# Kernel optimization log

Hardware: AMD Instinct MI355X
Metric: run time of the kernel (lower is better)

Reference implementation:

```python
import jax, jax.numpy as jnp
import numpy as np

N, X_DIM, Y_DIM, HID = 8192, 512, 2048 // 4, 2048
Y_DIM = 512

def setup_inputs() -> dict:
    key = jax.random.key(0)
    ks = jax.random.split(key, 10)
    def lin(k, fan_in, fan_out):
        lim = 1.0 / np.sqrt(fan_in)
        kw, kb = jax.random.split(k)
        W = jax.random.uniform(kw, (fan_in, fan_out), jnp.float32, -lim, lim)
        b = jax.random.uniform(kb, (fan_out,), jnp.float32, -lim, lim)
        return W, b
    mu_W1, mu_b1 = lin(ks[0], X_DIM, HID)
    mu_W2, mu_b2 = lin(ks[1], HID, Y_DIM)
    lv_W1, lv_b1 = lin(ks[2], X_DIM, HID)
    lv_W2, lv_b2 = lin(ks[3], HID, Y_DIM)
    return {
        "x_samples": jax.random.normal(ks[4], (N, X_DIM), jnp.float32),
        "y_samples": jax.random.normal(ks[5], (N, Y_DIM), jnp.float32),
        "mu_W1": mu_W1, "mu_b1": mu_b1, "mu_W2": mu_W2, "mu_b2": mu_b2,
        "lv_W1": lv_W1, "lv_b1": lv_b1, "lv_W2": lv_W2, "lv_b2": lv_b2,
    }

def reference(x_samples, y_samples, mu_W1, mu_b1, mu_W2, mu_b2, lv_W1, lv_b1, lv_W2, lv_b2):
    # MLP heads (GEMMs)
    mu = jax.nn.relu(x_samples @ mu_W1 + mu_b1) @ mu_W2 + mu_b2          # [N, D]
    logvar = jnp.tanh(jax.nn.relu(x_samples @ lv_W1 + lv_b1) @ lv_W2 + lv_b2)  # [N, D]
    w = 0.5 * jnp.exp(-logvar)                                           # 1/(2*exp(logvar))
    n = x_samples.shape[0]

    # positive: -mean_i sum_d (mu_id - y_id)^2 * w_id
    positive = -(((mu - y_samples) ** 2) * w).sum(axis=1).mean()

    # negative (exact decomposition of the [N,N,D] broadcast):
    # -(1/N^2) sum_{i,d} w_id * (N*mu_id^2 - 2*mu_id*Sy_d + Sy2_d)
    Sy = y_samples.sum(axis=0)          # [D]
    Sy2 = (y_samples ** 2).sum(axis=0)  # [D]
    negative = -(w * (n * mu ** 2 - 2.0 * mu * Sy + Sy2)).sum() / (n * n)

    return positive - negative
```

## Files before the change

### kernel.cpp

```cpp
#include <hip/hip_runtime.h>
#include <hip/hip_bf16.h>
#include <stdint.h>

#define NS   8192
#define XD   512
#define HD   2048
#define YD   512

typedef unsigned short u16;
using bf16x8 = __attribute__((ext_vector_type(8))) short;
using f32x4  = __attribute__((ext_vector_type(4))) float;

__device__ __forceinline__ float bf2f(u16 u) {
  union { uint32_t i; float f; } v; v.i = ((uint32_t)u) << 16; return v.f;
}
__device__ __forceinline__ u16 f2b(float f) {
  __hip_bfloat16 hb = __float2bfloat16(f);
  return *(const u16*)&hb;
}
__device__ __forceinline__ float ld_in(const void* p, int f32, size_t i) {
  return f32 ? ((const float*)p)[i] : bf2f(((const u16*)p)[i]);
}
#define GLDS(gp, lp) __builtin_amdgcn_global_load_lds( \
    (__attribute__((address_space(1))) void*)(gp),     \
    (__attribute__((address_space(3))) void*)(lp), 16, 0, 0)

__device__ __forceinline__ int probe_f32(const void* p, int n_u16, int* sflag) {
  if (threadIdx.x == 0) *sflag = 0;
  __syncthreads();
  const u16* q = (const u16*)p;
  int wild = 0;
  for (int i = threadIdx.x; i < n_u16; i += blockDim.x) {
    float v = bf2f(q[i]);
    if (!(fabsf(v) <= 1000.0f)) wild = 1;
  }
  if (wild) *sflag = 1;
  __syncthreads();
  int r = *sflag;
  __syncthreads();
  return r;
}

__global__ __launch_bounds__(256) void prep_all(
    const void* __restrict__ x,
    const void* w1m, const void* b1m, const void* w2m, const void* b2m,
    const void* w1l, const void* b1l, const void* w2l, const void* b2l,
    const void* __restrict__ y,
    u16* __restrict__ xb, float* __restrict__ biasv,
    u16* __restrict__ W1t, u16* __restrict__ W2tm, u16* __restrict__ W2tl,
    float* __restrict__ Sy, float* __restrict__ Sy2) {
  __shared__ u16 tile[64 * 72];
  __shared__ int sflag;
  const int b = blockIdx.x;
  const int tid = threadIdx.x;

  if (b < 2048) {
    if (!probe_f32(x, 1024, &sflag)) return;
    const size_t base = (size_t)b * 2048 + (size_t)tid * 8;
    alignas(16) u16 o[8];
    const float4* s = (const float4*)((const float*)x + base);
    float4 v0 = s[0], v1 = s[1];
    o[0]=f2b(v0.x); o[1]=f2b(v0.y); o[2]=f2b(v0.z); o[3]=f2b(v0.w);
    o[4]=f2b(v1.x); o[5]=f2b(v1.y); o[6]=f2b(v1.z); o[7]=f2b(v1.w);
    *(uint4*)(xb + base) = *(const uint4*)o;
  } else if (b == 2048) {
    const int f3 = probe_f32(b1m, 1024, &sflag);
    const int f5 = probe_f32(b2m, 512, &sflag);
    const int f7 = probe_f32(b1l, 1024, &sflag);
    const int f9 = probe_f32(b2l, 512, &sflag);
    for (int i = tid; i < 5120; i += 256) {
      float v;
      if (i < 2048)      v = ld_in(b1m, f3, i);
      else if (i < 4096) v = ld_in(b1l, f7, i - 2048);
      else if (i < 4608) v = ld_in(b2m, f5, i - 4096);
      else               v = ld_in(b2l, f9, i - 4608);
      biasv[i] = v;
    }
  } else if (b < 3073) {
    const int id = b - 2049, which = id >> 8, t = id & 255;
    const void* in; u16* out; int R, C;
    if (which == 0)      { in = w1m; out = W1t;                   R = XD; C = HD; }
    else if (which == 1) { in = w2m; out = W2tm;                  R = HD; C = YD; }
    else if (which == 2) { in = w1l; out = W1t + (size_t)HD * XD; R = XD; C = HD; }
    else                 { in = w2l; out = W2tl;                  R = HD; C = YD; }
    const int f = probe_f32(in, 1024, &sflag);
    const int nbx = C >> 6;
    const int c0 = (t % nbx) * 64, r0 = (t / nbx) * 64;
    const int r = tid >> 2, cc = (tid & 3) * 16;
    if (f) {
      const float4* s = (const float4*)((const float*)in + (size_t)(r0 + r) * C + c0 + cc);
#pragma unroll
      for (int k = 0; k < 4; ++k) {
        float4 v = s[k];
        tile[r * 72 + cc + k * 4 + 0] = f2b(v.x);
        tile[r * 72 + cc + k * 4 + 1] = f2b(v.y);
        tile[r * 72 + cc + k * 4 + 2] = f2b(v.z);
        tile[r * 72 + cc + k * 4 + 3] = f2b(v.w);
      }
    } else {
      const uint4* s = (const uint4*)((const u16*)in + (size_t)(r0 + r) * C + c0 + cc);
      *(uint4*)&tile[r * 72 + cc]     = s[0];
      *(uint4*)&tile[r * 72 + cc + 8] = s[1];
    }
    __syncthreads();
    const int i = tid >> 2, jc = (tid & 3) * 16;
    alignas(16) u16 o[16];
#pragma unroll
    for (int j = 0; j < 16; ++j) o[j] = tile[(jc + j) * 72 + i];
    uint4* dq = (uint4*)&out[(size_t)(c0 + i) * R + r0 + jc];
    dq[0] = ((const uint4*)o)[0];
    dq[1] = ((const uint4*)o)[1];
  } else {
    const int id2 = b - 3073;
    const int yf = probe_f32(y, 1024, &sflag);
    const int half = tid >> 7;
    const int c0 = (tid & 127) * 4;
    const int r0 = id2 * 128 + half * 64;
    float s0 = 0.f, s1 = 0.f, s2 = 0.f, s3 = 0.f;
    float q0 = 0.f, q1 = 0.f, q2 = 0.f, q3 = 0.f;
    for (int r = r0; r < r0 + 64; r += 4) {
#pragma unroll
      for (int rr = 0; rr < 4; ++rr) {
        float v0, v1, v2, v3;
        if (yf) {
          const float4 t4 = *(const float4*)((const float*)y + (size_t)(r + rr) * YD + c0);
          v0 = t4.x; v1 = t4.y; v2 = t4.z; v3 = t4.w;
        } else {
          const uint2 t2 = *(const uint2*)((const u16*)y + (size_t)(r + rr) * YD + c0);
          v0 = bf2f((u16)(t2.x & 0xffff)); v1 = bf2f((u16)(t2.x >> 16));
          v2 = bf2f((u16)(t2.y & 0xffff)); v3 = bf2f((u16)(t2.y >> 16));
        }
        s0 += v0; q0 += v0 * v0;  s1 += v1; q1 += v1 * v1;
        s2 += v2; q2 += v2 * v2;  s3 += v3; q3 += v3 * v3;
      }
    }
    atomicAdd(&Sy[c0],     s0);  atomicAdd(&Sy2[c0],     q0);
    atomicAdd(&Sy[c0 + 1], s1);  atomicAdd(&Sy2[c0 + 1], q1);
    atomicAdd(&Sy[c0 + 2], s2);  atomicAdd(&Sy2[c0 + 2], q2);
    atomicAdd(&Sy[c0 + 3], s3);  atomicAdd(&Sy2[c0 + 3], q3);
  }
}

#define SYNC_PRE do { \
  __builtin_amdgcn_sched_barrier(0); \
  __builtin_amdgcn_s_barrier(); \
  asm volatile("s_waitcnt lgkmcnt(0)" ::: "memory"); \
  __builtin_amdgcn_sched_barrier(0); \
  __builtin_amdgcn_s_setprio(1); } while (0)
#define SYNC_POST do { \
  __builtin_amdgcn_s_setprio(0); \
  __builtin_amdgcn_sched_barrier(0); \
  __builtin_amdgcn_s_barrier(); \
  __builtin_amdgcn_sched_barrier(0); } while (0)
#define VMCNT(N) asm volatile("s_waitcnt vmcnt(" #N ")" ::: "memory")
#define LGKM0 asm volatile("s_waitcnt lgkmcnt(0)" ::: "memory")
#define SCB __builtin_amdgcn_sched_barrier(0)

#define RD_A(MH, BUF) do { \
  const u16* ab_ = &lds[((BUF)*2 + wm) * 8192]; \
  _Pragma("unroll") for (int q_ = 0; q_ < 4; ++q_) \
    _Pragma("unroll") for (int ks_ = 0; ks_ < 2; ++ks_) \
      af[q_][ks_] = *(const bf16x8*)&ab_[((MH)*64 + q_*16 + c16)*64 + (((ks_*4+quad) ^ cswz) << 3)]; \
} while (0)

#define RD_B(NH, BUF) do { \
  const u16* bb_ = &lds[32768 + ((BUF)*2 + (wn>>1)) * 8192]; \
  _Pragma("unroll") for (int p_ = 0; p_ < 2; ++p_) \
    _Pragma("unroll") for (int ks_ = 0; ks_ < 2; ++ks_) \
      bf[(NH)*2+p_][ks_] = *(const bf16x8*)&bb_[((wn&1)*64 + ((NH)*2+p_)*16 + c16)*64 + (((ks_*4+quad) ^ cswz) << 3)]; \
} while (0)

#define MM(MH, NH) do { \
  _Pragma("unroll") for (int ks_ = 0; ks_ < 2; ++ks_) \
    _Pragma("unroll") for (int q_ = 0; q_ < 4; ++q_) \
      _Pragma("unroll") for (int p_ = 0; p_ < 2; ++p_) \
        acc[(MH)*4+q_][(NH)*2+p_] = __builtin_amdgcn_mfma_f32_16x16x32_bf16( \
            af[q_][ks_], bf[(NH)*2+p_][ks_], acc[(MH)*4+q_][(NH)*2+p_], 0, 0, 0); \
} while (0)

#define ST_A(KT, HALF) do { if ((KT) < 8) { \
  u16* lb_ = &lds[(((KT)&1)*2 + (HALF))*8192 + (wid << 9)]; \
  const u16* sp_ = Aptr + (size_t)(bm0 + (HALF)*128 + (wid<<3) + srow)*512 + ((KT)<<6) + scg; \
  GLDS(sp_, lb_); GLDS(sp_ + (size_t)64*512, lb_ + 4096); } } while (0)

#define ST_B(KT, HALF) do { if ((KT) < 8) { \
  u16* lb_ = &lds[32768 + (((KT)&1)*2 + (HALF))*8192 + (wid << 9)]; \
  const u16* sp_ = W1t + (size_t)(bn0 + (HALF)*128 + (wid<<3) + srow)*512 + ((KT)<<6) + scg; \
  GLDS(sp_, lb_); GLDS(sp_ + (size_t)64*512, lb_ + 4096); } } while (0)

__global__ __launch_bounds__(512, 2) void gemm1_kernel(
    const void* __restrict__ xraw, const u16* __restrict__ xb,
    const u16* __restrict__ W1t,
    const float* __restrict__ bias,
    u16* __restrict__ h_mu, u16* __restrict__ h_lv) {
  __shared__ alignas(16) u16 lds[65536];
  __shared__ int sflag;
  const int tid = threadIdx.x;

  const u16* Aptr = probe_f32(xraw, 1024, &sflag) ? xb : (const u16*)xraw;

  const int wid = tid >> 6, lane = tid & 63;
  const int wm = wid >> 2, wn = wid & 3;
  const int quad = lane >> 4, c16 = lane & 15, cswz = c16 & 7;
  const int srow = lane >> 3;
  const int scg  = ((lane & 7) ^ srow) << 3;

  const int id = blockIdx.x;
  const int xcd = id & 7, slot = id >> 3;
  const int bm0 = (xcd * 4 + (slot & 3)) * 256;
  const int bn0 = (slot >> 2) * 256;

  f32x4 acc[8][4] = {};
  bf16x8 af[4][2], bf[4][2];

  ST_B(0, 0); ST_B(0, 1); ST_A(0, 0); ST_A(0, 1);
  ST_B(1, 0); ST_B(1, 1);
  VMCNT(4);
  __builtin_amdgcn_s_barrier();
  __builtin_amdgcn_sched_barrier(0);

#pragma unroll
  for (int i = 0; i < 4; ++i) {
    const int ka = 2 * i, kb = ka + 1;
    const bool last = (i == 3);
    RD_A(0, 0); RD_B(0, 0); ST_A(kb, 0);
    SYNC_PRE; MM(0, 0); SYNC_POST;
    RD_B(1, 0); ST_A(kb, 1);
    SYNC_PRE; MM(0, 1); SYNC_POST;
    RD_A(1, 0); ST_B(ka + 2, 0);
    SYNC_PRE; MM(1, 0); SYNC_POST;
    ST_B(ka + 2, 1);
    SYNC_PRE; MM(1, 1);
    if (!last) { VMCNT(4); } else { VMCNT(0); }
    SYNC_POST;
    RD_A(0, 1); RD_B(0, 1); ST_A(ka + 2, 0);
    SYNC_PRE; MM(0, 0); SYNC_POST;
    RD_B(1, 1); ST_A(ka + 2, 1);
    SYNC_PRE; MM(0, 1); SYNC_POST;
    RD_A(1, 1); ST_B(kb + 2, 0);
    SYNC_PRE; MM(1, 0); SYNC_POST;
    ST_B(kb + 2, 1);
    SYNC_PRE; MM(1, 1);
    if (!last) { VMCNT(4); }
    SYNC_POST;
  }

  u16* myl = &lds[wid * 8192];
  const bool is_lv = bn0 >= HD;
  u16* dst = is_lv ? h_lv : h_mu;
  const int wncol = wn << 6;
  const int gc0 = (bn0 - (is_lv ? HD : 0)) + wncol;
  const int grow0 = bm0 + (wm << 7);
#pragma unroll
  for (int ni = 0; ni < 4; ++ni) {
    const float bv = bias[bn0 + wncol + ni * 16 + c16];
#pragma unroll
    for (int mi = 0; mi < 8; ++mi)
#pragma unroll
      for (int r = 0; r < 4; ++r) {
        const int row = mi * 16 + (quad << 2) + r;
        const int col = ni * 16 + c16;
        myl[row * 64 + ((((col >> 3) ^ (row & 7)) << 3) | (col & 7))] =
            f2b(fmaxf(acc[mi][ni][r] + bv, 0.f));
      }
  }
#pragma unroll
  for (int it = 0; it < 16; ++it) {
    const int row = (it << 3) + (lane >> 3);
    const int ch = lane & 7;
    const uint4 v = *(const uint4*)&myl[row * 64 + ((ch ^ (row & 7)) << 3)];
    *(uint4*)&dst[(size_t)(grow0 + row) * HD + gc0 + (ch << 3)] = v;
  }
}

#undef RD_A
#undef RD_B
#undef MM
#undef ST_A
#undef ST_B

#define LDA8(AF, T) do { \
  const uint64_t o_ = (uint64_t)(T) * 128u; \
  asm volatile("global_load_dwordx4 %0, %1, off"           : "=v"(AF[0][0]) : "v"(aA[0] + o_)); \
  asm volatile("global_load_dwordx4 %0, %1, off offset:64" : "=v"(AF[0][1]) : "v"(aA[0] + o_)); \
  asm volatile("global_load_dwordx4 %0, %1, off"           : "=v"(AF[1][0]) : "v"(aA[1] + o_)); \
  asm volatile("global_load_dwordx4 %0, %1, off offset:64" : "=v"(AF[1][1]) : "v"(aA[1] + o_)); \
  asm volatile("global_load_dwordx4 %0, %1, off"           : "=v"(AF[2][0]) : "v"(aA[2] + o_)); \
  asm volatile("global_load_dwordx4 %0, %1, off offset:64" : "=v"(AF[2][1]) : "v"(aA[2] + o_)); \
  asm volatile("global_load_dwordx4 %0, %1, off"           : "=v"(AF[3][0]) : "v"(aA[3] + o_)); \
  asm volatile("global_load_dwordx4 %0, %1, off offset:64" : "=v"(AF[3][1]) : "v"(aA[3] + o_)); \
} while (0)

#define RD8(BUFI) do { \
  _Pragma("unroll") for (int ni_ = 0; ni_ < 4; ++ni_) \
    _Pragma("unroll") for (int ks_ = 0; ks_ < 2; ++ks_) \
      bf[ni_][ks_] = *(const bf16x8*)&lds[(BUFI)*16384 + rbase + \
          (wn*64 + ni_*16 + c16)*64 + (((ks_*4+quad) ^ cswz) << 3)]; \
} while (0)

#define MM32(AF) do { \
  _Pragma("unroll") for (int ks_ = 0; ks_ < 2; ++ks_) \
    _Pragma("unroll") for (int mi_ = 0; mi_ < 4; ++mi_) \
      _Pragma("unroll") for (int ni_ = 0; ni_ < 4; ++ni_) \
        acc[mi_][ni_] = __builtin_amdgcn_mfma_f32_16x16x32_bf16( \
            AF[mi_][ks_], bf[ni_][ks_], acc[mi_][ni_], 0, 0, 0); \
} while (0)

#define STB2(KT, BI) do { \
  u16* lbm_ = lds + (BI)*16384 + (wid << 9); \
  const u16* spm_ = bMp + (size_t)(KT)*64; \
  GLDS(spm_, lbm_); GLDS(spm_ + (size_t)64*HD, lbm_ + 4096); \
  u16* lbl_ = lbm_ + 8192; \
  const u16* spl_ = bLp + (size_t)(KT)*64; \
  GLDS(spl_, lbl_); GLDS(spl_ + (size_t)64*HD, lbl_ + 4096); \
} while (0)

#define PH6(T, AFc, AFn, BR, BS) do { \
  SCB; RD8(BR); SCB; \
  LDA8(AFn, (T) + 1); SCB; \
  STB2((T) + 2, BS); SCB; \
  LGKM0; SCB; \
  VMCNT(12); SCB; \
  __builtin_amdgcn_s_barrier(); SCB; \
  __builtin_amdgcn_s_setprio(1); \
  MM32(AFc); \
  __builtin_amdgcn_s_setprio(0); SCB; \
} while (0)

__global__ __launch_bounds__(512, 2) void gemm2_dual(
    const u16* __restrict__ hm, const u16* __restrict__ hl,
    const u16* __restrict__ W2m, const u16* __restrict__ W2l,
    const float* __restrict__ b2m, const float* __restrict__ b2l,
    const void* __restrict__ y,
    const float* __restrict__ Sy, const float* __restrict__ Sy2,
    double* __restrict__ gacc, unsigned* __restrict__ counter,
    float* __restrict__ out) {
  __shared__ alignas(16) u16 lds[49152];
  __shared__ double bs[8];
  __shared__ int sflag;

  const int yf = probe_f32(y, 1024, &sflag);

  const int tid = threadIdx.x, wid = tid >> 6, lane = tid & 63;
  const int wh = wid >> 2;
  const int wm = (wid >> 1) & 1, wn = wid & 1;
  const int quad = lane >> 4, c16 = lane & 15, cswz = c16 & 7;
  const int srow = lane >> 3;
  const int scg  = ((lane & 7) ^ srow) << 3;
  const int rbase = wh * 8192;

  const int id = blockIdx.x;
  const int xcd = id & 7, slot = id >> 3;
  const int bm0 = (xcd * 8 + (slot >> 2)) * 128;
  const int bn0 = (slot & 3) * 128;

  const u16* bMp = W2m + (size_t)(bn0 + (wid << 3) + srow) * HD + scg;
  const u16* bLp = W2l + (size_t)(bn0 + (wid << 3) + srow) * HD + scg;

  const u16* hx = wh ? hl : hm;
  uint64_t aA[4];
#pragma unroll
  for (int mi = 0; mi < 4; ++mi)
    aA[mi] = (uint64_t)(uintptr_t)(
        hx + (size_t)(bm0 + wm * 64 + mi * 16 + c16) * HD + quad * 8);

  f32x4 acc[4][4] = {};
  bf16x8 afA[4][2], afB[4][2], bf[4][2];

  STB2(0, 0); STB2(1, 1);
  SCB;
  LDA8(afA, 0);
  SCB;
  VMCNT(12);
  __builtin_amdgcn_s_barrier();
  SCB;

#pragma unroll 1
  for (int i = 0; i < 5; ++i) {
    PH6(6 * i + 0, afA, afB, 0, 2);
    PH6(6 * i + 1, afB, afA, 1, 0);
    PH6(6 * i + 2, afA, afB, 2, 1);
    PH6(6 * i + 3, afB, afA, 0, 2);
    PH6(6 * i + 4, afA, afB, 1, 0);
    PH6(6 * i + 5, afB, afA, 2, 1);
  }
  SCB; RD8(0); SCB;
  LDA8(afB, 31); SCB;
  LGKM0; SCB;
  VMCNT(8);
  SCB;
  __builtin_amdgcn_s_barrier(); SCB;
  __builtin_amdgcn_s_setprio(1);
  MM32(afA);
  __builtin_amdgcn_s_setprio(0); SCB;
  RD8(1); SCB;
  LGKM0; SCB;
  VMCNT(0);
  SCB;
  __builtin_amdgcn_s_setprio(1);
  MM32(afB);
  __builtin_amdgcn_s_setprio(0);

  __syncthreads();
  float* ldsF = (float*)lds;
  float* mur = ldsF + (wid & 3) * 4224;
  if (wh == 0) {
#pragma unroll
    for (int ni = 0; ni < 4; ++ni) {
      const float bmv = b2m[bn0 + wn * 64 + ni * 16 + c16];
#pragma unroll
      for (int mi = 0; mi < 4; ++mi)
#pragma unroll
        for (int r = 0; r < 4; ++r)
          mur[(mi * 16 + quad * 4 + r) * 66 + ni * 16 + c16] =
              acc[mi][ni][r] + bmv;
    }
  }
  __syncthreads();
  const float invN = 1.0f / (float)NS;
  float s = 0.f;
  if (wh == 1) {
#pragma unroll
    for (int ni = 0; ni < 4; ++ni) {
      const int gcol = bn0 + wn * 64 + ni * 16 + c16;
      const float blv = b2l[gcol];
      const float syv = Sy[gcol], sy2v = Sy2[gcol];
#pragma unroll
      for (int mi = 0; mi < 4; ++mi)
#pragma unroll
        for (int r = 0; r < 4; ++r) {
          const int grow = bm0 + wm * 64 + mi * 16 + quad * 4 + r;
          const float m   = mur[(mi * 16 + quad * 4 + r) * 66 + ni * 16 + c16];
          const float lvp = acc[mi][ni][r] + blv;
          const float w   = 0.5f * expf(-tanhf(lvp));
          const float yv  = ld_in(y, yf, (size_t)grow * YD + gcol);
          s += w * (yv * yv - 2.f * m * yv + (2.f * m * syv - sy2v) * invN);
        }
    }
  }
  for (int off = 32; off > 0; off >>= 1) s += __shfl_down(s, off);
  if (lane == 0) bs[wid] = (double)s;
  __syncthreads();
  if (tid == 0) {
    atomicAdd(gacc, bs[0] + bs[1] + bs[2] + bs[3] +
                    bs[4] + bs[5] + bs[6] + bs[7]);
    __threadfence();
    const unsigned old = atomicAdd(counter, 1u);
    if (old == gridDim.x - 1) {
      const double g = atomicAdd(gacc, 0.0);
      out[0] = (float)(-g / (double)NS);
    }
  }
}

extern "C" void kernel_launch(void* const* d_in, const int* in_sizes, int n_in,
                              void* d_out, int out_size, void* d_ws, size_t ws_size,
                              hipStream_t stream) {
  char* ws = (char*)d_ws;
  double*   gacc    = (double*)ws;
  unsigned* counter = (unsigned*)(ws + 8);
  float*    Sy      = (float*)(ws + 128);
  float*    Sy2     = (float*)(ws + 2176);
  float*    biasv   = (float*)(ws + 4224);
  u16* xb   = (u16*)(ws + 24704);
  u16* W1t  = xb + (size_t)NS * XD;
  u16* W2tm = W1t + (size_t)2 * HD * XD;
  u16* W2tl = W2tm + (size_t)YD * HD;
  u16* h_mu = W2tl + (size_t)YD * HD;
  u16* h_lv = h_mu + (size_t)NS * HD;

  hipMemsetAsync(d_ws, 0, 4224, stream);

  prep_all<<<2049 + 1024 + 64, 256, 0, stream>>>(
      d_in[0], d_in[2], d_in[3], d_in[4], d_in[5],
      d_in[6], d_in[7], d_in[8], d_in[9], d_in[1],
      xb, biasv, W1t, W2tm, W2tl, Sy, Sy2);

  const float* b1  = biasv;
  const float* b2m = biasv + 4096, *b2l = biasv + 4608;

  gemm1_kernel<<<(NS / 256) * ((2 * HD) / 256), 512, 0, stream>>>(
      d_in[0], xb, W1t, b1, h_mu, h_lv);

  gemm2_dual<<<(NS / 128) * (YD / 128), 512, 0, stream>>>(
      h_mu, h_lv, W2tm, W2tl, b2m, b2l, d_in[1], Sy, Sy2,
      gacc, counter, (float*)d_out);
}
```

Baseline: 261.4 us.

## Split A-fragment loads into half-K stages to cut register double-buffering in gemm2

The second GEMM's main loop stops double-buffering full A fragments in registers (afA/afB). Each K tile is now split into two k-halves: the MFMA for one half runs, then the next tile's matching half of A is loaded into the freed registers, with finer vmcnt/lgkmcnt waits in between. The aim is to lower VGPR pressure and overlap global A loads with MFMA work at a finer grain. The cost is a shorter prefetch distance for A, which could expose global-load latency before the next MFMA batch.

```diff
diff --git a/kernel.cpp b/kernel.cpp
--- a/kernel.cpp
+++ b/kernel.cpp
@@ -153,7 +153,7 @@
   __builtin_amdgcn_s_barrier(); \
   __builtin_amdgcn_sched_barrier(0); } while (0)
 #define VMCNT(N) asm volatile("s_waitcnt vmcnt(" #N ")" ::: "memory")
-#define LGKM0 asm volatile("s_waitcnt lgkmcnt(0)" ::: "memory")
+#define LGKM(N) asm volatile("s_waitcnt lgkmcnt(" #N ")" ::: "memory")
 #define SCB __builtin_amdgcn_sched_barrier(0)
 
 #define RD_A(MH, BUF) do { \
@@ -279,31 +279,33 @@
 #undef ST_A
 #undef ST_B
 
-#define LDA8(AF, T) do { \
+#define LDA4LO(T) do { \
   const uint64_t o_ = (uint64_t)(T) * 128u; \
-  asm volatile("global_load_dwordx4 %0, %1, off"           : "=v"(AF[0][0]) : "v"(aA[0] + o_)); \
-  asm volatile("global_load_dwordx4 %0, %1, off offset:64" : "=v"(AF[0][1]) : "v"(aA[0] + o_)); \
-  asm volatile("global_load_dwordx4 %0, %1, off"           : "=v"(AF[1][0]) : "v"(aA[1] + o_)); \
-  asm volatile("global_load_dwordx4 %0, %1, off offset:64" : "=v"(AF[1][1]) : "v"(aA[1] + o_)); \
-  asm volatile("global_load_dwordx4 %0, %1, off"           : "=v"(AF[2][0]) : "v"(aA[2] + o_)); \
-  asm volatile("global_load_dwordx4 %0, %1, off offset:64" : "=v"(AF[2][1]) : "v"(aA[2] + o_)); \
-  asm volatile("global_load_dwordx4 %0, %1, off"           : "=v"(AF[3][0]) : "v"(aA[3] + o_)); \
-  asm volatile("global_load_dwordx4 %0, %1, off offset:64" : "=v"(AF[3][1]) : "v"(aA[3] + o_)); \
-} while (0)
-
-#define RD8(BUFI) do { \
+  asm volatile("global_load_dwordx4 %0, %1, off" : "=v"(afLo[0]) : "v"(aA[0] + o_)); \
+  asm volatile("global_load_dwordx4 %0, %1, off" : "=v"(afLo[1]) : "v"(aA[1] + o_)); \
+  asm volatile("global_load_dwordx4 %0, %1, off" : "=v"(afLo[2]) : "v"(aA[2] + o_)); \
+  asm volatile("global_load_dwordx4 %0, %1, off" : "=v"(afLo[3]) : "v"(aA[3] + o_)); \
+} while (0)
+
+#define LDA4HI(T) do { \
+  const uint64_t o_ = (uint64_t)(T) * 128u; \
+  asm volatile("global_load_dwordx4 %0, %1, off offset:64" : "=v"(afHi[0]) : "v"(aA[0] + o_)); \
+  asm volatile("global_load_dwordx4 %0, %1, off offset:64" : "=v"(afHi[1]) : "v"(aA[1] + o_)); \
+  asm volatile("global_load_dwordx4 %0, %1, off offset:64" : "=v"(afHi[2]) : "v"(aA[2] + o_)); \
+  asm volatile("global_load_dwordx4 %0, %1, off offset:64" : "=v"(afHi[3]) : "v"(aA[3] + o_)); \
+} while (0)
+
+#define RD4(BF, BUFI, KS) do { \
   _Pragma("unroll") for (int ni_ = 0; ni_ < 4; ++ni_) \
-    _Pragma("unroll") for (int ks_ = 0; ks_ < 2; ++ks_) \
-      bf[ni_][ks_] = *(const bf16x8*)&lds[(BUFI)*16384 + rbase + \
-          (wn*64 + ni_*16 + c16)*64 + (((ks_*4+quad) ^ cswz) << 3)]; \
-} while (0)
-
-#define MM32(AF) do { \
-  _Pragma("unroll") for (int ks_ = 0; ks_ < 2; ++ks_) \
-    _Pragma("unroll") for (int mi_ = 0; mi_ < 4; ++mi_) \
-      _Pragma("unroll") for (int ni_ = 0; ni_ < 4; ++ni_) \
-        acc[mi_][ni_] = __builtin_amdgcn_mfma_f32_16x16x32_bf16( \
-            AF[mi_][ks_], bf[ni_][ks_], acc[mi_][ni_], 0, 0, 0); \
+    BF[ni_] = *(const bf16x8*)&lds[(BUFI)*16384 + rbase + \
+        (wn*64 + ni_*16 + c16)*64 + ((((KS)*4+quad) ^ cswz) << 3)]; \
+} while (0)
+
+#define MM16(AF, BF) do { \
+  _Pragma("unroll") for (int mi_ = 0; mi_ < 4; ++mi_) \
+    _Pragma("unroll") for (int ni_ = 0; ni_ < 4; ++ni_) \
+      acc[mi_][ni_] = __builtin_amdgcn_mfma_f32_16x16x32_bf16( \
+          AF[mi_], BF[ni_], acc[mi_][ni_], 0, 0, 0); \
 } while (0)
 
 #define STB2(KT, BI) do { \
@@ -315,16 +317,16 @@
   GLDS(spl_, lbl_); GLDS(spl_ + (size_t)64*HD, lbl_ + 4096); \
 } while (0)
 
-#define PH6(T, AFc, AFn, BR, BS) do { \
-  SCB; RD8(BR); SCB; \
-  LDA8(AFn, (T) + 1); SCB; \
+#define PH7(T, BR, BS) do { \
+  SCB; RD4(bfLo, BR, 0); RD4(bfHi, BR, 1); SCB; \
   STB2((T) + 2, BS); SCB; \
-  LGKM0; SCB; \
-  VMCNT(12); SCB; \
+  VMCNT(8); LGKM(4); SCB; \
+  __builtin_amdgcn_s_setprio(1); MM16(afLo, bfLo); __builtin_amdgcn_s_setprio(0); SCB; \
+  LDA4LO((T) + 1); SCB; \
+  VMCNT(8); LGKM(0); SCB; \
+  __builtin_amdgcn_s_setprio(1); MM16(afHi, bfHi); __builtin_amdgcn_s_setprio(0); SCB; \
+  LDA4HI((T) + 1); SCB; \
   __builtin_amdgcn_s_barrier(); SCB; \
-  __builtin_amdgcn_s_setprio(1); \
-  MM32(AFc); \
-  __builtin_amdgcn_s_setprio(0); SCB; \
 } while (0)
 
 __global__ __launch_bounds__(512, 2) void gemm2_dual(
@@ -365,41 +367,35 @@
         hx + (size_t)(bm0 + wm * 64 + mi * 16 + c16) * HD + quad * 8);
 
   f32x4 acc[4][4] = {};
-  bf16x8 afA[4][2], afB[4][2], bf[4][2];
+  bf16x8 afLo[4], afHi[4], bfLo[4], bfHi[4];
 
   STB2(0, 0); STB2(1, 1);
   SCB;
-  LDA8(afA, 0);
+  LDA4LO(0); LDA4HI(0);
   SCB;
   VMCNT(12);
   __builtin_amdgcn_s_barrier();
   SCB;
 
 #pragma unroll 1
-  for (int i = 0; i < 5; ++i) {
-    PH6(6 * i + 0, afA, afB, 0, 2);
-    PH6(6 * i + 1, afB, afA, 1, 0);
-    PH6(6 * i + 2, afA, afB, 2, 1);
-    PH6(6 * i + 3, afB, afA, 0, 2);
-    PH6(6 * i + 4, afA, afB, 1, 0);
-    PH6(6 * i + 5, afB, afA, 2, 1);
-  }
-  SCB; RD8(0); SCB;
-  LDA8(afB, 31); SCB;
-  LGKM0; SCB;
-  VMCNT(8);
-  SCB;
+  for (int i = 0; i < 10; ++i) {
+    PH7(3 * i + 0, 0, 2);
+    PH7(3 * i + 1, 1, 0);
+    PH7(3 * i + 2, 2, 1);
+  }
+  SCB; RD4(bfLo, 0, 0); RD4(bfHi, 0, 1); SCB;
+  VMCNT(4); LGKM(4); SCB;
+  __builtin_amdgcn_s_setprio(1); MM16(afLo, bfLo); __builtin_amdgcn_s_setprio(0); SCB;
+  LDA4LO(31); SCB;
+  VMCNT(4); LGKM(0); SCB;
+  __builtin_amdgcn_s_setprio(1); MM16(afHi, bfHi); __builtin_amdgcn_s_setprio(0); SCB;
+  LDA4HI(31); SCB;
   __builtin_amdgcn_s_barrier(); SCB;
-  __builtin_amdgcn_s_setprio(1);
-  MM32(afA);
-  __builtin_amdgcn_s_setprio(0); SCB;
-  RD8(1); SCB;
-  LGKM0; SCB;
-  VMCNT(0);
-  SCB;
-  __builtin_amdgcn_s_setprio(1);
-  MM32(afB);
-  __builtin_amdgcn_s_setprio(0);
+  RD4(bfLo, 1, 0); RD4(bfHi, 1, 1); SCB;
+  VMCNT(4); LGKM(4); SCB;
+  __builtin_amdgcn_s_setprio(1); MM16(afLo, bfLo); __builtin_amdgcn_s_setprio(0); SCB;
+  VMCNT(0); LGKM(0); SCB;
+  __builtin_amdgcn_s_setprio(1); MM16(afHi, bfHi); __builtin_amdgcn_s_setprio(0);
 
   __syncthreads();
   float* ldsF = (float*)lds;
```

New measurement: 259.0 us. About the same (-0.9%).
